# Kernel optimization log

Hardware: AMD Instinct MI355X
Metric: run time of the kernel (lower is better)

The kernel has to match this reference:

```python
import jax, jax.numpy as jnp
import numpy as np

N_NODES = 50000
N_EDGES = 800000
IN_F, HID, EMB = 10, 256, 128
BN_EPS = 1e-5


def _glorot(key, shape):
    fan_in, fan_out = shape[0], shape[1]
    lim = (6.0 / (fan_in + fan_out)) ** 0.5
    return jax.random.uniform(key, shape, jnp.float32, -lim, lim)


def setup_inputs() -> dict:
    key = jax.random.key(0)
    ks = jax.random.split(key, 16)
    inp = {
        "x": jax.random.normal(ks[0], (N_NODES, IN_F), jnp.float32),
        "edge_index": jax.random.randint(ks[1], (2, N_EDGES), 0, N_NODES, jnp.int64),
        # input_proj: Linear(10,256) + BN
        "w_in": _glorot(ks[2], (IN_F, HID)),
        "b_in": jnp.zeros((HID,), jnp.float32),
        "g_in": jnp.ones((HID,), jnp.float32),
        "be_in": jnp.zeros((HID,), jnp.float32),
        # SAGEConv 1 (256->256): lin_l (neighbor aggr, with bias), lin_r (root, no bias)
        "wl1": _glorot(ks[3], (HID, HID)), "bl1": jnp.zeros((HID,), jnp.float32), "wr1": _glorot(ks[4], (HID, HID)),
        "g1": jnp.ones((HID,), jnp.float32), "be1": jnp.zeros((HID,), jnp.float32),
        # SAGEConv 2 (256->256)
        "wl2": _glorot(ks[5], (HID, HID)), "bl2": jnp.zeros((HID,), jnp.float32), "wr2": _glorot(ks[6], (HID, HID)),
        "g2": jnp.ones((HID,), jnp.float32), "be2": jnp.zeros((HID,), jnp.float32),
        # SAGEConv 3 (256->128)
        "wl3": _glorot(ks[7], (HID, EMB)), "bl3": jnp.zeros((EMB,), jnp.float32), "wr3": _glorot(ks[8], (HID, EMB)),
    }
    return inp


def _bn(h, g, b):
    # BatchNorm1d in training-mode math (batch statistics, biased variance)
    mu = jnp.mean(h, axis=0)
    var = jnp.var(h, axis=0)
    return (h - mu) * jax.lax.rsqrt(var + BN_EPS) * g + b


def _sage(h, src, dst, wl, bl, wr):
    # mean aggregation of neighbor messages: gather h[src], scatter-mean into dst
    msg = h[src]                                             # [E, d]
    s = jax.ops.segment_sum(msg, dst, num_segments=N_NODES)  # [N, d]
    cnt = jax.ops.segment_sum(jnp.ones((msg.shape[0],), h.dtype), dst, num_segments=N_NODES)
    agg = s / jnp.maximum(cnt, 1.0)[:, None]                 # isolated nodes -> 0
    return agg @ wl + bl + h @ wr


def reference(x, edge_index, w_in, b_in, g_in, be_in,
              wl1, bl1, wr1, g1, be1,
              wl2, bl2, wr2, g2, be2,
              wl3, bl3, wr3):
    src, dst = edge_index[0], edge_index[1]
    # input_proj: Linear + BN + ReLU (dropout disabled for determinism)
    h = jax.nn.relu(_bn(x @ w_in + b_in, g_in, be_in))
    h = jax.nn.relu(_bn(_sage(h, src, dst, wl1, bl1, wr1), g1, be1))
    h = jax.nn.relu(_bn(_sage(h, src, dst, wl2, bl2, wr2), g2, be2))
    h = _sage(h, src, dst, wl3, bl3, wr3)
    return h
```

## Files before the change

### kernel.cpp

```cpp
#include <hip/hip_runtime.h>

#define N_NODES 50000
#define N_EDGES 800000
#define IN_F 10
#define HID 256
#define EMB 128
#define BN_EPS 1e-5f
#define N_SCAN_BLKS ((N_NODES + 255) / 256)
#define CNT_BLKS (N_EDGES / 256)
#define WCONV_ELEMS (4 * HID * HID + 2 * EMB * HID)
#define WCONV_BLKS (WCONV_ELEMS / 256)
#define SSTRIDE 512
#define NSHARD 8
#define NPART 8
#define PART_SZ (N_NODES / NPART)
#define SCAT_BLKS 2048

typedef __attribute__((ext_vector_type(8))) short short8;
typedef __attribute__((ext_vector_type(4))) float floatx4;
typedef __attribute__((ext_vector_type(2))) float floatx2;

__device__ __forceinline__ unsigned short f2bf(float f) {
    unsigned u = __float_as_uint(f);
    unsigned r = (u + 0x7fffu + ((u >> 16) & 1u)) >> 16;
    return (unsigned short)r;
}
__device__ __forceinline__ float bf_lo(unsigned int u) { return __uint_as_float(u << 16); }
__device__ __forceinline__ float bf_hi(unsigned int u) { return __uint_as_float(u & 0xffff0000u); }
__device__ __forceinline__ float bf2f(unsigned short s) { return __uint_as_float(((unsigned)s) << 16); }

__device__ __forceinline__ void gload_lds16(const unsigned short* g, unsigned short* l) {
    __builtin_amdgcn_global_load_lds(
        (const __attribute__((address_space(1))) unsigned int*)(uintptr_t)(const void*)g,
        (__attribute__((address_space(3))) unsigned int*)(unsigned int)(uintptr_t)(void*)l,
        16, 0, 0);
}

__global__ void k_count_wconv(const int* __restrict__ e_dst, int* __restrict__ cnt,
                              const float* __restrict__ wl1, const float* __restrict__ wr1,
                              const float* __restrict__ wl2, const float* __restrict__ wr2,
                              const float* __restrict__ wl3, const float* __restrict__ wr3,
                              unsigned short* __restrict__ wl1t, unsigned short* __restrict__ wr1t,
                              unsigned short* __restrict__ wl2t, unsigned short* __restrict__ wr2t,
                              unsigned short* __restrict__ wl3t, unsigned short* __restrict__ wr3t) {
    int b = blockIdx.x;
    int t = threadIdx.x;
    if (b < CNT_BLKS) {
        atomicAdd(&cnt[e_dst[b * 256 + t]], 1);
        return;
    }
    int idx = (b - CNT_BLKS) * 256 + t;
    const int S = HID * HID;
    if (idx < 4 * S) {
        int sel = idx >> 16;
        int o = idx & (S - 1);
        const float* w = sel == 0 ? wl1 : sel == 1 ? wr1 : sel == 2 ? wl2 : wr2;
        unsigned short* wt = sel == 0 ? wl1t : sel == 1 ? wr1t : sel == 2 ? wl2t : wr2t;
        int n = o >> 8, k = o & 255;
        wt[o] = f2bf(w[k * HID + n]);
    } else {
        int r = idx - 4 * S;
        int sel = r >> 15;
        int o = r & 32767;
        const float* w = sel ? wr3 : wl3;
        unsigned short* wt = sel ? wr3t : wl3t;
        int n = o >> 8, k = o & 255;
        wt[o] = f2bf(w[k * EMB + n]);
    }
}

__global__ void k_reduce_cnt(const int* __restrict__ cnt, int* __restrict__ part) {
    __shared__ int sdata[256];
    int i = blockIdx.x * 256 + threadIdx.x;
    sdata[threadIdx.x] = (i < N_NODES) ? cnt[i] : 0;
    __syncthreads();
    for (int off = 128; off > 0; off >>= 1) {
        if (threadIdx.x < off) sdata[threadIdx.x] += sdata[threadIdx.x + off];
        __syncthreads();
    }
    if (threadIdx.x == 0) part[blockIdx.x] = sdata[0];
}

__global__ void k_scan_part(const int* __restrict__ part, int* __restrict__ partoff,
                            int* __restrict__ row_off_last) {
    __shared__ int buf[256];
    int tid = threadIdx.x;
    int v = (tid < N_SCAN_BLKS) ? part[tid] : 0;
    buf[tid] = v;
    __syncthreads();
    for (int off = 1; off < 256; off <<= 1) {
        int t = (tid >= off) ? buf[tid - off] : 0;
        __syncthreads();
        buf[tid] += t;
        __syncthreads();
    }
    if (tid < N_SCAN_BLKS) partoff[tid] = buf[tid] - v;
    if (tid == 255) *row_off_last = buf[255];
}

__global__ void k_scan_final(const int* __restrict__ cnt, const int* __restrict__ partoff,
                             int* __restrict__ row_off, int* __restrict__ fill_pos) {
    __shared__ int buf[256];
    int tid = threadIdx.x;
    int i = blockIdx.x * 256 + tid;
    int v = (i < N_NODES) ? cnt[i] : 0;
    buf[tid] = v;
    __syncthreads();
    for (int off = 1; off < 256; off <<= 1) {
        int t = (tid >= off) ? buf[tid - off] : 0;
        __syncthreads();
        buf[tid] += t;
        __syncthreads();
    }
    if (i < N_NODES) {
        int excl = partoff[blockIdx.x] + buf[tid] - v;
        row_off[i] = excl;
        fill_pos[i] = excl;
    }
}

__global__ void k_scatter_part(const int* __restrict__ src, const int* __restrict__ dst,
                               int* __restrict__ fill_pos, int* __restrict__ sorted_src) {
    int part = blockIdx.x & 7;
    int lo = part * PART_SZ, hi = lo + PART_SZ;
    int idx = (blockIdx.x >> 3) * 256 + threadIdx.x;
    for (int e = idx; e < N_EDGES; e += (SCAT_BLKS / 8) * 256) {
        int d = dst[e];
        if (d >= lo && d < hi) {
            int p = atomicAdd(&fill_pos[d], 1);
            sorted_src[p] = src[e];
        }
    }
}

#define IP_BLOCKS 1024
__global__ __launch_bounds__(256) void k_input_proj(
        const float* __restrict__ x, const float* __restrict__ w,
        const float* __restrict__ bias, unsigned short* __restrict__ h,
        float* __restrict__ stats) {
    __shared__ float sbuf[2048];
    __shared__ float qbuf[2048];
    int t = threadIdx.x;
    int jg = t & 31;
    int ns = t >> 5;
    int j0 = jg * 8;

    float wreg[IN_F][8];
#pragma unroll
    for (int k = 0; k < IN_F; k++)
#pragma unroll
        for (int c = 0; c < 8; c++) wreg[k][c] = w[k * HID + j0 + c];
    float bj[8];
#pragma unroll
    for (int c = 0; c < 8; c++) bj[c] = bias[j0 + c];

    float s[8] = {}, q[8] = {};
    const int stride = IP_BLOCKS * 8;
    for (int base = blockIdx.x * 8 + ns; base < N_NODES; base += stride) {
        float xr[IN_F];
#pragma unroll
        for (int k = 0; k < IN_F; k++) xr[k] = x[base * IN_F + k];
        float acc[8];
#pragma unroll
        for (int c = 0; c < 8; c++) {
            float a = bj[c];
#pragma unroll
            for (int k = 0; k < IN_F; k++) a += xr[k] * wreg[k][c];
            acc[c] = a;
            s[c] += a;
            q[c] += a * a;
        }
        uint4 o;
        o.x = (unsigned)f2bf(acc[0]) | ((unsigned)f2bf(acc[1]) << 16);
        o.y = (unsigned)f2bf(acc[2]) | ((unsigned)f2bf(acc[3]) << 16);
        o.z = (unsigned)f2bf(acc[4]) | ((unsigned)f2bf(acc[5]) << 16);
        o.w = (unsigned)f2bf(acc[6]) | ((unsigned)f2bf(acc[7]) << 16);
        ((uint4*)h)[(size_t)base * 32 + jg] = o;
    }

#pragma unroll
    for (int c = 0; c < 8; c++) {
        sbuf[ns * 256 + j0 + c] = s[c];
        qbuf[ns * 256 + j0 + c] = q[c];
    }
    __syncthreads();
    float ss = 0.f, qq = 0.f;
#pragma unroll
    for (int n2 = 0; n2 < 8; n2++) {
        ss += sbuf[n2 * 256 + t];
        qq += qbuf[n2 * 256 + t];
    }
    atomicAdd(&stats[t], ss);
    atomicAdd(&stats[256 + t], qq);
}

__global__ void k_bn_apply_relu(unsigned short* __restrict__ h, const float* __restrict__ stats,
                                const float* __restrict__ g, const float* __restrict__ b,
                                unsigned char* __restrict__ h8) {
    int idx = blockIdx.x * 256 + threadIdx.x;
    if (idx >= N_NODES * 32) return;
    int q = idx & 31;
    int j0 = q * 8;
    const float invn = 1.0f / (float)N_NODES;
    float sc[8], sh[8];
#pragma unroll
    for (int k = 0; k < 8; k++) {
        float ssum = 0.f, qsum = 0.f;
#pragma unroll
        for (int s = 0; s < NSHARD; s++) {
            ssum += stats[s * SSTRIDE + j0 + k];
            qsum += stats[s * SSTRIDE + 256 + j0 + k];
        }
        float mu = ssum * invn;
        float var = qsum * invn - mu * mu;
        float scale = g[j0 + k] * rsqrtf(var + BN_EPS);
        sc[k] = scale;
        sh[k] = b[j0 + k] - mu * scale;
    }
    uint4 v = ((uint4*)h)[idx];
    float f0 = fmaxf(bf_lo(v.x) * sc[0] + sh[0], 0.f);
    float f1 = fmaxf(bf_hi(v.x) * sc[1] + sh[1], 0.f);
    float f2 = fmaxf(bf_lo(v.y) * sc[2] + sh[2], 0.f);
    float f3 = fmaxf(bf_hi(v.y) * sc[3] + sh[3], 0.f);
    float f4 = fmaxf(bf_lo(v.z) * sc[4] + sh[4], 0.f);
    float f5 = fmaxf(bf_hi(v.z) * sc[5] + sh[5], 0.f);
    float f6 = fmaxf(bf_lo(v.w) * sc[6] + sh[6], 0.f);
    float f7 = fmaxf(bf_hi(v.w) * sc[7] + sh[7], 0.f);
    uint4 o;
    o.x = (unsigned)f2bf(f0) | ((unsigned)f2bf(f1) << 16);
    o.y = (unsigned)f2bf(f2) | ((unsigned)f2bf(f3) << 16);
    o.z = (unsigned)f2bf(f4) | ((unsigned)f2bf(f5) << 16);
    o.w = (unsigned)f2bf(f6) | ((unsigned)f2bf(f7) << 16);
    ((uint4*)h)[idx] = o;
    if (h8) {
        unsigned pa = __builtin_amdgcn_cvt_pk_fp8_f32(f0, f1, 0u, false);
        pa = __builtin_amdgcn_cvt_pk_fp8_f32(f2, f3, pa, true);
        unsigned pb = __builtin_amdgcn_cvt_pk_fp8_f32(f4, f5, 0u, false);
        pb = __builtin_amdgcn_cvt_pk_fp8_f32(f6, f7, pb, true);
        uint2 o8; o8.x = pa; o8.y = pb;
        ((uint2*)h8)[idx] = o8;
    }
}

__global__ void k_aggregate_fp8(const unsigned char* __restrict__ h8,
                                const int* __restrict__ row_off, const int* __restrict__ cnt,
                                const int* __restrict__ sorted_src,
                                unsigned short* __restrict__ agg) {
    int node = (blockIdx.x * blockDim.x + threadIdx.x) >> 4;
    int lane = threadIdx.x & 15;
    if (node >= N_NODES) return;
    int beg = row_off[node];
    int d = cnt[node];
    int end = beg + d;
    const uint4* h4 = (const uint4*)h8;
    float a[16] = {};
    for (int e = beg; e < end; e++) {
        int s = sorted_src[e];
        uint4 v = h4[(size_t)s * 16 + lane];
        floatx2 p;
        p = __builtin_amdgcn_cvt_pk_f32_fp8(v.x, false); a[0] += p.x;  a[1] += p.y;
        p = __builtin_amdgcn_cvt_pk_f32_fp8(v.x, true);  a[2] += p.x;  a[3] += p.y;
        p = __builtin_amdgcn_cvt_pk_f32_fp8(v.y, false); a[4] += p.x;  a[5] += p.y;
        p = __builtin_amdgcn_cvt_pk_f32_fp8(v.y, true);  a[6] += p.x;  a[7] += p.y;
        p = __builtin_amdgcn_cvt_pk_f32_fp8(v.z, false); a[8] += p.x;  a[9] += p.y;
        p = __builtin_amdgcn_cvt_pk_f32_fp8(v.z, true);  a[10] += p.x; a[11] += p.y;
        p = __builtin_amdgcn_cvt_pk_f32_fp8(v.w, false); a[12] += p.x; a[13] += p.y;
        p = __builtin_amdgcn_cvt_pk_f32_fp8(v.w, true);  a[14] += p.x; a[15] += p.y;
    }
    float inv = 1.0f / (float)(d > 1 ? d : 1);
    uint4 o0, o1;
    o0.x = (unsigned)f2bf(a[0] * inv)  | ((unsigned)f2bf(a[1] * inv) << 16);
    o0.y = (unsigned)f2bf(a[2] * inv)  | ((unsigned)f2bf(a[3] * inv) << 16);
    o0.z = (unsigned)f2bf(a[4] * inv)  | ((unsigned)f2bf(a[5] * inv) << 16);
    o0.w = (unsigned)f2bf(a[6] * inv)  | ((unsigned)f2bf(a[7] * inv) << 16);
    o1.x = (unsigned)f2bf(a[8] * inv)  | ((unsigned)f2bf(a[9] * inv) << 16);
    o1.y = (unsigned)f2bf(a[10] * inv) | ((unsigned)f2bf(a[11] * inv) << 16);
    o1.z = (unsigned)f2bf(a[12] * inv) | ((unsigned)f2bf(a[13] * inv) << 16);
    o1.w = (unsigned)f2bf(a[14] * inv) | ((unsigned)f2bf(a[15] * inv) << 16);
    ((uint4*)agg)[(size_t)node * 32 + lane * 2] = o0;
    ((uint4*)agg)[(size_t)node * 32 + lane * 2 + 1] = o1;
}

__global__ void k_aggregate_add(const unsigned short* __restrict__ G, const int* __restrict__ row_off,
                                const int* __restrict__ cnt, const int* __restrict__ sorted_src,
                                float* __restrict__ out) {
    int node = (blockIdx.x * blockDim.x + threadIdx.x) >> 4;
    int lane = threadIdx.x & 15;
    if (node >= N_NODES) return;
    int beg = row_off[node];
    int d = cnt[node];
    int end = beg + d;
    const uint4* h4 = (const uint4*)G;
    float a0 = 0.f, a1 = 0.f, a2 = 0.f, a3 = 0.f, a4 = 0.f, a5 = 0.f, a6 = 0.f, a7 = 0.f;
    for (int e = beg; e < end; e++) {
        int s = sorted_src[e];
        uint4 v = h4[(size_t)s * 16 + lane];
        a0 += bf_lo(v.x); a1 += bf_hi(v.x);
        a2 += bf_lo(v.y); a3 += bf_hi(v.y);
        a4 += bf_lo(v.z); a5 += bf_hi(v.z);
        a6 += bf_lo(v.w); a7 += bf_hi(v.w);
    }
    float inv = 1.0f / (float)(d > 1 ? d : 1);
    float4* ob = (float4*)(out + (size_t)node * EMB + lane * 8);
    float4 p0 = ob[0], p1 = ob[1];
    p0.x += a0 * inv; p0.y += a1 * inv; p0.z += a2 * inv; p0.w += a3 * inv;
    p1.x += a4 * inv; p1.y += a5 * inv; p1.z += a6 * inv; p1.w += a7 * inv;
    ob[0] = p0; ob[1] = p1;
}

#define BK 64

#define GEMM_BLKS 784

template <int NCOL, bool STATS>
__global__ __launch_bounds__(512, 4) void k_gemm_mfma(
        const unsigned short* __restrict__ A1, const unsigned short* __restrict__ B1t,
        const unsigned short* __restrict__ A2, const unsigned short* __restrict__ B2t,
        const float* __restrict__ bias, float* __restrict__ stats,
        unsigned short* __restrict__ Cout) {
    int b = blockIdx.x;
    int xcd = b & 7;
    int q = b >> 3;
    int cx = q & 1;
    int pr = (q >> 1) * 8 + xcd;
    int r0 = pr * 128;
    if (r0 >= N_NODES) return;
    int c0 = cx * 128;

    __shared__ __attribute__((aligned(16))) unsigned short As[2][128 * 64];
    __shared__ __attribute__((aligned(16))) unsigned short Bs[2][128 * 64];

    int t = threadIdx.x;
    int wave = t >> 6, lane = t & 63;
    int wm = wave >> 2, wn = wave & 3;
    int quad = lane >> 4, l15 = lane & 15;

    floatx4 acc[4][2];
#pragma unroll
    for (int i = 0; i < 4; i++)
#pragma unroll
        for (int j = 0; j < 2; j++) acc[i][j] = (floatx4){0.f, 0.f, 0.f, 0.f};

    auto stage = [&](int buf, const unsigned short* __restrict__ A,
                     const unsigned short* __restrict__ B, int k0) {
#pragma unroll
        for (int it = 0; it < 2; it++) {
            int p = it * 512 + t;
            int row = p >> 3, ps = p & 7;
            int ls = ps ^ (row & 7);
            int rr = r0 + row;
            if (rr >= N_NODES) rr = N_NODES - 1;
            gload_lds16(&A[(size_t)rr * HID + k0 + ls * 8], &As[buf][p * 8]);
        }
#pragma unroll
        for (int it = 0; it < 2; it++) {
            int p = it * 512 + t;
            int row = p >> 3, ps = p & 7;
            int ls = ps ^ (row & 7);
            gload_lds16(&B[(size_t)(c0 + row) * HID + k0 + ls * 8], &Bs[buf][p * 8]);
        }
    };

    stage(0, A1, B1t, 0);

    int cur = 0;
#pragma unroll
    for (int ph = 0; ph < 8; ph++) {
        if (ph < 7) {
            int np = ph + 1;
            stage(cur ^ 1, (np >= 4) ? A2 : A1, (np >= 4) ? B2t : B1t, (np & 3) * BK);
            asm volatile("s_waitcnt vmcnt(4)\n\ts_barrier" ::: "memory");
        } else {
            asm volatile("s_waitcnt vmcnt(0)\n\ts_barrier" ::: "memory");
        }
#pragma unroll
        for (int kc = 0; kc < 2; kc++) {
            short8 a[4], bfr[2];
            int ls = kc * 4 + quad;
#pragma unroll
            for (int i = 0; i < 4; i++) {
                int arow = wm * 64 + i * 16 + l15;
                int ps = ls ^ (arow & 7);
                a[i] = *(const short8*)&As[cur][arow * 64 + ps * 8];
            }
#pragma unroll
            for (int j = 0; j < 2; j++) {
                int brow = wn * 32 + j * 16 + l15;
                int ps = ls ^ (brow & 7);
                bfr[j] = *(const short8*)&Bs[cur][brow * 64 + ps * 8];
            }
            __builtin_amdgcn_s_setprio(1);
#pragma unroll
            for (int i = 0; i < 4; i++)
#pragma unroll
                for (int j = 0; j < 2; j++)
                    acc[i][j] = __builtin_amdgcn_mfma_f32_16x16x32_bf16(a[i], bfr[j], acc[i][j], 0, 0, 0);
            __builtin_amdgcn_s_setprio(0);
        }
        asm volatile("s_barrier" ::: "memory");
        cur ^= 1;
    }

    float bv[2];
#pragma unroll
    for (int j = 0; j < 2; j++) bv[j] = bias[c0 + wn * 32 + j * 16 + l15];

    float s_part[2] = {0.f, 0.f};
    float q_part[2] = {0.f, 0.f};

#pragma unroll
    for (int i = 0; i < 4; i++) {
#pragma unroll
        for (int r = 0; r < 4; r++) {
            int m = r0 + wm * 64 + i * 16 + quad * 4 + r;
            if (m >= N_NODES) continue;
#pragma unroll
            for (int j = 0; j < 2; j++) {
                int n = c0 + wn * 32 + j * 16 + l15;
                float v = acc[i][j][r] + bv[j];
                if (STATS) { s_part[j] += v; q_part[j] += v * v; }
                Cout[(size_t)m * NCOL + n] = f2bf(v);
            }
        }
    }

    if (STATS) {
        float* sred = (float*)As;
        __syncthreads();
        if (t < 256) sred[t] = 0.f;
        __syncthreads();
#pragma unroll
        for (int j = 0; j < 2; j++) {
            int cl = wn * 32 + j * 16 + l15;
            atomicAdd(&sred[cl], s_part[j]);
            atomicAdd(&sred[128 + cl], q_part[j]);
        }
        __syncthreads();
        if (t < 128) {
            int base = (pr & (NSHARD - 1)) * SSTRIDE;
            atomicAdd(&stats[base + c0 + t], sred[t]);
            atomicAdd(&stats[base + 256 + c0 + t], sred[128 + t]);
        }
    }
}

#define L3_BLKS 784

__global__ __launch_bounds__(512, 4) void k_gemm_l3_dual(
        const unsigned short* __restrict__ A, const unsigned short* __restrict__ Bt,
        const float* __restrict__ stats,
        const float* __restrict__ g, const float* __restrict__ be,
        const float* __restrict__ bl3, unsigned short* __restrict__ G,
        float* __restrict__ P) {
    int b = blockIdx.x;
    int xcd = b & 7;
    int q = b >> 3;
    int cx = q & 1;
    int pr = (q >> 1) * 8 + xcd;
    int r0 = pr * 128;
    if (r0 >= N_NODES) return;
    int c0 = cx * 128;

    __shared__ __attribute__((aligned(16))) unsigned short As[128 * 64];
    __shared__ __attribute__((aligned(16))) unsigned short Bs[2][128 * 64];
    __shared__ float scs[256], shs[256];

    int t = threadIdx.x;
    if (t < 256) {
        const float invn = 1.0f / (float)N_NODES;
        float ssum = 0.f, qsum = 0.f;
#pragma unroll
        for (int s = 0; s < NSHARD; s++) {
            ssum += stats[s * SSTRIDE + t];
            qsum += stats[s * SSTRIDE + 256 + t];
        }
        float mu = ssum * invn;
        float var = qsum * invn - mu * mu;
        float sc = g[t] * rsqrtf(var + BN_EPS);
        scs[t] = sc;
        shs[t] = be[t] - mu * sc;
    }
    __syncthreads();

    int wave = t >> 6, lane = t & 63;
    int wm = wave >> 2, wn = wave & 3;
    int quad = lane >> 4, l15 = lane & 15;

    floatx4 acc[4][2];
#pragma unroll
    for (int i = 0; i < 4; i++)
#pragma unroll
        for (int j = 0; j < 2; j++) acc[i][j] = (floatx4){0.f, 0.f, 0.f, 0.f};

    int p0_ = t, p1_ = 512 + t;
    int row0 = p0_ >> 3, ps0 = p0_ & 7, ls0 = ps0 ^ (row0 & 7);
    int row1 = p1_ >> 3, ps1 = p1_ & 7, ls1 = ps1 ^ (row1 & 7);
    int ar0 = r0 + row0; if (ar0 >= N_NODES) ar0 = N_NODES - 1;
    int ar1 = r0 + row1; if (ar1 >= N_NODES) ar1 = N_NODES - 1;

    auto stageB = [&](int buf, int k0) {
        gload_lds16(&Bt[(size_t)(c0 + row0) * HID + k0 + ls0 * 8], &Bs[buf][p0_ * 8]);
        gload_lds16(&Bt[(size_t)(c0 + row1) * HID + k0 + ls1 * 8], &Bs[buf][p1_ * 8]);
    };
    auto issueA = [&](int k0, uint4& v0, uint4& v1) {
        v0 = *(const uint4*)&A[(size_t)ar0 * HID + k0 + ls0 * 8];
        v1 = *(const uint4*)&A[(size_t)ar1 * HID + k0 + ls1 * 8];
    };
    auto xform = [&](uint4 vv, int cb) -> uint4 {
        float4 s0 = *(float4*)&scs[cb], s1 = *(float4*)&scs[cb + 4];
        float4 h0 = *(float4*)&shs[cb], h1 = *(float4*)&shs[cb + 4];
        float f0 = fmaxf(bf_lo(vv.x) * s0.x + h0.x, 0.f);
        float f1 = fmaxf(bf_hi(vv.x) * s0.y + h0.y, 0.f);
        float f2 = fmaxf(bf_lo(vv.y) * s0.z + h0.z, 0.f);
        float f3 = fmaxf(bf_hi(vv.y) * s0.w + h0.w, 0.f);
        float f4 = fmaxf(bf_lo(vv.z) * s1.x + h1.x, 0.f);
        float f5 = fmaxf(bf_hi(vv.z) * s1.y + h1.y, 0.f);
        float f6 = fmaxf(bf_lo(vv.w) * s1.z + h1.z, 0.f);
        float f7 = fmaxf(bf_hi(vv.w) * s1.w + h1.w, 0.f);
        uint4 ov;
        ov.x = (unsigned)f2bf(f0) | ((unsigned)f2bf(f1) << 16);
        ov.y = (unsigned)f2bf(f2) | ((unsigned)f2bf(f3) << 16);
        ov.z = (unsigned)f2bf(f4) | ((unsigned)f2bf(f5) << 16);
        ov.w = (unsigned)f2bf(f6) | ((unsigned)f2bf(f7) << 16);
        return ov;
    };

    uint4 va0, va1, vb0, vb1;
    stageB(0, 0);
    issueA(0, va0, va1);

    int cur = 0;
#pragma unroll
    for (int ph = 0; ph < 4; ph++) {
        if (ph < 3) {
            stageB(cur ^ 1, (ph + 1) * BK);
            asm volatile("s_waitcnt vmcnt(2)" ::: "memory");
        } else {
            asm volatile("s_waitcnt vmcnt(0)" ::: "memory");
        }
        *(uint4*)&As[p0_ * 8] = xform(va0, ph * BK + ls0 * 8);
        *(uint4*)&As[p1_ * 8] = xform(va1, ph * BK + ls1 * 8);
        asm volatile("s_waitcnt lgkmcnt(0)\n\ts_barrier" ::: "memory");
        if (ph < 3) issueA((ph + 1) * BK, vb0, vb1);
#pragma unroll
        for (int kc = 0; kc < 2; kc++) {
            short8 a[4], bfr[2];
            int ls = kc * 4 + quad;
#pragma unroll
            for (int i = 0; i < 4; i++) {
                int arow = wm * 64 + i * 16 + l15;
                int ps = ls ^ (arow & 7);
                a[i] = *(const short8*)&As[arow * 64 + ps * 8];
            }
#pragma unroll
            for (int j = 0; j < 2; j++) {
                int brow = wn * 32 + j * 16 + l15;
                int ps = ls ^ (brow & 7);
                bfr[j] = *(const short8*)&Bs[cur][brow * 64 + ps * 8];
            }
            __builtin_amdgcn_s_setprio(1);
#pragma unroll
            for (int i = 0; i < 4; i++)
#pragma unroll
                for (int j = 0; j < 2; j++)
                    acc[i][j] = __builtin_amdgcn_mfma_f32_16x16x32_bf16(a[i], bfr[j], acc[i][j], 0, 0, 0);
            __builtin_amdgcn_s_setprio(0);
        }
        asm volatile("s_barrier" ::: "memory");
        cur ^= 1;
        va0 = vb0; va1 = vb1;
    }

    float bv[2];
#pragma unroll
    for (int j = 0; j < 2; j++) bv[j] = bl3[wn * 32 + j * 16 + l15];

#pragma unroll
    for (int i = 0; i < 4; i++) {
#pragma unroll
        for (int r = 0; r < 4; r++) {
            int m = r0 + wm * 64 + i * 16 + quad * 4 + r;
            if (m >= N_NODES) continue;
#pragma unroll
            for (int j = 0; j < 2; j++) {
                int n = wn * 32 + j * 16 + l15;
                if (cx == 0) G[(size_t)m * EMB + n] = f2bf(acc[i][j][r]);
                else         P[(size_t)m * EMB + n] = acc[i][j][r] + bv[j];
            }
        }
    }
}

extern "C" void kernel_launch(void* const* d_in, const int* in_sizes, int n_in,
                              void* d_out, int out_size, void* d_ws, size_t ws_size,
                              hipStream_t stream) {
    const float* x    = (const float*)d_in[0];
    const int*   ei   = (const int*)d_in[1];
    const float* w_in = (const float*)d_in[2];
    const float* b_in = (const float*)d_in[3];
    const float* g_in = (const float*)d_in[4];
    const float* be_in= (const float*)d_in[5];
    const float* wl1  = (const float*)d_in[6];
    const float* bl1  = (const float*)d_in[7];
    const float* wr1  = (const float*)d_in[8];
    const float* g1   = (const float*)d_in[9];
    const float* be1  = (const float*)d_in[10];
    const float* wl2  = (const float*)d_in[11];
    const float* bl2  = (const float*)d_in[12];
    const float* wr2  = (const float*)d_in[13];
    const float* g2   = (const float*)d_in[14];
    const float* be2  = (const float*)d_in[15];
    const float* wl3  = (const float*)d_in[16];
    const float* bl3  = (const float*)d_in[17];
    const float* wr3  = (const float*)d_in[18];
    float* out = (float*)d_out;

    char* p = (char*)d_ws;
    auto alloc = [&](size_t bytes) -> void* {
        void* r = (void*)p;
        p += (bytes + 255) & ~(size_t)255;
        return r;
    };
    int*   cnt    = (int*)alloc((size_t)N_NODES * 4);
    float* stats0 = (float*)alloc((size_t)NSHARD * SSTRIDE * 4);
    float* stats1 = (float*)alloc((size_t)NSHARD * SSTRIDE * 4);
    float* stats2 = (float*)alloc((size_t)NSHARD * SSTRIDE * 4);
    size_t zlen = (size_t)((char*)stats2 + NSHARD * SSTRIDE * 4 - (char*)cnt);

    unsigned short* bufA = (unsigned short*)alloc((size_t)N_NODES * HID * 2);
    unsigned short* bufB = (unsigned short*)alloc((size_t)N_NODES * HID * 2);
    unsigned short* bufC = (unsigned short*)alloc((size_t)N_NODES * HID * 2);
    unsigned char*  h8   = (unsigned char*)alloc((size_t)N_NODES * HID);
    unsigned short* wl1t = (unsigned short*)alloc((size_t)HID * HID * 2);
    unsigned short* wr1t = (unsigned short*)alloc((size_t)HID * HID * 2);
    unsigned short* wl2t = (unsigned short*)alloc((size_t)HID * HID * 2);
    unsigned short* wr2t = (unsigned short*)alloc((size_t)HID * HID * 2);
    unsigned short* wl3t = (unsigned short*)alloc((size_t)EMB * HID * 2);
    unsigned short* wr3t = (unsigned short*)alloc((size_t)EMB * HID * 2);
    int*   row_off    = (int*)alloc((size_t)(N_NODES + 1) * 4);
    int*   fill_pos   = (int*)alloc((size_t)N_NODES * 4);
    int*   sorted_src = (int*)alloc((size_t)N_EDGES * 4);
    int*   part       = (int*)alloc((size_t)256 * 4);
    int*   partoff    = (int*)alloc((size_t)256 * 4);
    (void)wr3t;

    const int* e_src = ei;
    const int* e_dst = ei + N_EDGES;

    hipMemsetAsync(cnt, 0, zlen, stream);
    k_count_wconv<<<CNT_BLKS + WCONV_BLKS, 256, 0, stream>>>(
        e_dst, cnt, wl1, wr1, wl2, wr2, wl3, wr3, wl1t, wr1t, wl2t, wr2t, wl3t, wr3t);
    k_reduce_cnt<<<N_SCAN_BLKS, 256, 0, stream>>>(cnt, part);
    k_scan_part<<<1, 256, 0, stream>>>(part, partoff, &row_off[N_NODES]);
    k_scan_final<<<N_SCAN_BLKS, 256, 0, stream>>>(cnt, partoff, row_off, fill_pos);
    k_scatter_part<<<SCAT_BLKS, 256, 0, stream>>>(e_src, e_dst, fill_pos, sorted_src);

    k_input_proj<<<IP_BLOCKS, 256, 0, stream>>>(x, w_in, b_in, bufA, stats0);
    k_bn_apply_relu<<<(N_NODES * 32 + 255) / 256, 256, 0, stream>>>(bufA, stats0, g_in, be_in, h8);

    int aggF8_blocks = (N_NODES * 16 + 255) / 256;

    k_aggregate_fp8<<<aggF8_blocks, 256, 0, stream>>>(h8, row_off, cnt, sorted_src, bufC);
    k_gemm_mfma<HID, true><<<GEMM_BLKS, 512, 0, stream>>>(bufC, wl1t, bufA, wr1t, bl1, stats1, bufB);
    k_bn_apply_relu<<<(N_NODES * 32 + 255) / 256, 256, 0, stream>>>(bufB, stats1, g1, be1, h8);

    k_aggregate_fp8<<<aggF8_blocks, 256, 0, stream>>>(h8, row_off, cnt, sorted_src, bufC);
    k_gemm_mfma<HID, true><<<GEMM_BLKS, 512, 0, stream>>>(bufC, wl2t, bufB, wr2t, bl2, stats2, bufA);

    k_gemm_l3_dual<<<L3_BLKS, 512, 0, stream>>>(
        bufA, wl3t, stats2, g2, be2, bl3, bufB, out);
    k_aggregate_add<<<(N_NODES * 16 + 255) / 256, 256, 0, stream>>>(bufB, row_off, cnt, sorted_src, out);
}
```

Baseline: 486.1 us.

## Split aggregation edges across four lane groups and fuse input projection into count kernel

The aggregation kernels now assign a full 64-lane wavefront per node, with four 16-lane groups each handling every fourth edge, and combine the partial sums with cross-lane shuffles. This raises memory-level parallelism for the gathers over an average degree of 16 and spreads work more evenly across nodes with different degrees. Separately, the input projection is folded into the edge-count and weight-conversion launch as extra blocks, removing one kernel launch and letting that work overlap with the counting. The cost is four times as many threads per node, some of them idle for low-degree nodes, plus the shuffle reduction.

```diff
diff --git a/kernel.cpp b/kernel.cpp
--- a/kernel.cpp
+++ b/kernel.cpp
@@ -10,6 +10,7 @@
 #define CNT_BLKS (N_EDGES / 256)
 #define WCONV_ELEMS (4 * HID * HID + 2 * EMB * HID)
 #define WCONV_BLKS (WCONV_ELEMS / 256)
+#define IP_BLOCKS 1024
 #define SSTRIDE 512
 #define NSHARD 8
 #define NPART 8
@@ -36,37 +37,98 @@
         16, 0, 0);
 }
 
-__global__ void k_count_wconv(const int* __restrict__ e_dst, int* __restrict__ cnt,
-                              const float* __restrict__ wl1, const float* __restrict__ wr1,
-                              const float* __restrict__ wl2, const float* __restrict__ wr2,
-                              const float* __restrict__ wl3, const float* __restrict__ wr3,
-                              unsigned short* __restrict__ wl1t, unsigned short* __restrict__ wr1t,
-                              unsigned short* __restrict__ wl2t, unsigned short* __restrict__ wr2t,
-                              unsigned short* __restrict__ wl3t, unsigned short* __restrict__ wr3t) {
+__global__ __launch_bounds__(256) void k_count_wconv_ip(
+        const int* __restrict__ e_dst, int* __restrict__ cnt,
+        const float* __restrict__ wl1, const float* __restrict__ wr1,
+        const float* __restrict__ wl2, const float* __restrict__ wr2,
+        const float* __restrict__ wl3, const float* __restrict__ wr3,
+        unsigned short* __restrict__ wl1t, unsigned short* __restrict__ wr1t,
+        unsigned short* __restrict__ wl2t, unsigned short* __restrict__ wr2t,
+        unsigned short* __restrict__ wl3t, unsigned short* __restrict__ wr3t,
+        const float* __restrict__ x, const float* __restrict__ w,
+        const float* __restrict__ bias, unsigned short* __restrict__ h,
+        float* __restrict__ stats) {
+    __shared__ float sbuf[2048];
+    __shared__ float qbuf[2048];
     int b = blockIdx.x;
     int t = threadIdx.x;
     if (b < CNT_BLKS) {
         atomicAdd(&cnt[e_dst[b * 256 + t]], 1);
         return;
     }
-    int idx = (b - CNT_BLKS) * 256 + t;
-    const int S = HID * HID;
-    if (idx < 4 * S) {
-        int sel = idx >> 16;
-        int o = idx & (S - 1);
-        const float* w = sel == 0 ? wl1 : sel == 1 ? wr1 : sel == 2 ? wl2 : wr2;
-        unsigned short* wt = sel == 0 ? wl1t : sel == 1 ? wr1t : sel == 2 ? wl2t : wr2t;
-        int n = o >> 8, k = o & 255;
-        wt[o] = f2bf(w[k * HID + n]);
-    } else {
-        int r = idx - 4 * S;
-        int sel = r >> 15;
-        int o = r & 32767;
-        const float* w = sel ? wr3 : wl3;
-        unsigned short* wt = sel ? wr3t : wl3t;
-        int n = o >> 8, k = o & 255;
-        wt[o] = f2bf(w[k * EMB + n]);
-    }
+    if (b < CNT_BLKS + WCONV_BLKS) {
+        int idx = (b - CNT_BLKS) * 256 + t;
+        const int S = HID * HID;
+        if (idx < 4 * S) {
+            int sel = idx >> 16;
+            int o = idx & (S - 1);
+            const float* wp = sel == 0 ? wl1 : sel == 1 ? wr1 : sel == 2 ? wl2 : wr2;
+            unsigned short* wt = sel == 0 ? wl1t : sel == 1 ? wr1t : sel == 2 ? wl2t : wr2t;
+            int n = o >> 8, k = o & 255;
+            wt[o] = f2bf(wp[k * HID + n]);
+        } else {
+            int r = idx - 4 * S;
+            int sel = r >> 15;
+            int o = r & 32767;
+            const float* wp = sel ? wr3 : wl3;
+            unsigned short* wt = sel ? wr3t : wl3t;
+            int n = o >> 8, k = o & 255;
+            wt[o] = f2bf(wp[k * EMB + n]);
+        }
+        return;
+    }
+    int bb = b - CNT_BLKS - WCONV_BLKS;
+    int jg = t & 31;
+    int ns = t >> 5;
+    int j0 = jg * 8;
+
+    float wreg[IN_F][8];
+#pragma unroll
+    for (int k = 0; k < IN_F; k++)
+#pragma unroll
+        for (int c = 0; c < 8; c++) wreg[k][c] = w[k * HID + j0 + c];
+    float bj[8];
+#pragma unroll
+    for (int c = 0; c < 8; c++) bj[c] = bias[j0 + c];
+
+    float s[8] = {}, q[8] = {};
+    const int stride = IP_BLOCKS * 8;
+    for (int base = bb * 8 + ns; base < N_NODES; base += stride) {
+        float xr[IN_F];
+#pragma unroll
+        for (int k = 0; k < IN_F; k++) xr[k] = x[base * IN_F + k];
+        float acc[8];
+#pragma unroll
+        for (int c = 0; c < 8; c++) {
+            float a = bj[c];
+#pragma unroll
+            for (int k = 0; k < IN_F; k++) a += xr[k] * wreg[k][c];
+            acc[c] = a;
+            s[c] += a;
+            q[c] += a * a;
+        }
+        uint4 o;
+        o.x = (unsigned)f2bf(acc[0]) | ((unsigned)f2bf(acc[1]) << 16);
+        o.y = (unsigned)f2bf(acc[2]) | ((unsigned)f2bf(acc[3]) << 16);
+        o.z = (unsigned)f2bf(acc[4]) | ((unsigned)f2bf(acc[5]) << 16);
+        o.w = (unsigned)f2bf(acc[6]) | ((unsigned)f2bf(acc[7]) << 16);
+        ((uint4*)h)[(size_t)base * 32 + jg] = o;
+    }
+
+#pragma unroll
+    for (int c = 0; c < 8; c++) {
+        sbuf[ns * 256 + j0 + c] = s[c];
+        qbuf[ns * 256 + j0 + c] = q[c];
+    }
+    __syncthreads();
+    float ss = 0.f, qq = 0.f;
+#pragma unroll
+    for (int n2 = 0; n2 < 8; n2++) {
+        ss += sbuf[n2 * 256 + t];
+        qq += qbuf[n2 * 256 + t];
+    }
+    atomicAdd(&stats[t], ss);
+    atomicAdd(&stats[256 + t], qq);
 }
 
 __global__ void k_reduce_cnt(const int* __restrict__ cnt, int* __restrict__ part) {
@@ -131,67 +193,6 @@
             sorted_src[p] = src[e];
         }
     }
-}
-
-#define IP_BLOCKS 1024
-__global__ __launch_bounds__(256) void k_input_proj(
-        const float* __restrict__ x, const float* __restrict__ w,
-        const float* __restrict__ bias, unsigned short* __restrict__ h,
-        float* __restrict__ stats) {
-    __shared__ float sbuf[2048];
-    __shared__ float qbuf[2048];
-    int t = threadIdx.x;
-    int jg = t & 31;
-    int ns = t >> 5;
-    int j0 = jg * 8;
-
-    float wreg[IN_F][8];
-#pragma unroll
-    for (int k = 0; k < IN_F; k++)
-#pragma unroll
-        for (int c = 0; c < 8; c++) wreg[k][c] = w[k * HID + j0 + c];
-    float bj[8];
-#pragma unroll
-    for (int c = 0; c < 8; c++) bj[c] = bias[j0 + c];
-
-    float s[8] = {}, q[8] = {};
-    const int stride = IP_BLOCKS * 8;
-    for (int base = blockIdx.x * 8 + ns; base < N_NODES; base += stride) {
-        float xr[IN_F];
-#pragma unroll
-        for (int k = 0; k < IN_F; k++) xr[k] = x[base * IN_F + k];
-        float acc[8];
-#pragma unroll
-        for (int c = 0; c < 8; c++) {
-            float a = bj[c];
-#pragma unroll
-            for (int k = 0; k < IN_F; k++) a += xr[k] * wreg[k][c];
-            acc[c] = a;
-            s[c] += a;
-            q[c] += a * a;
-        }
-        uint4 o;
-        o.x = (unsigned)f2bf(acc[0]) | ((unsigned)f2bf(acc[1]) << 16);
-        o.y = (unsigned)f2bf(acc[2]) | ((unsigned)f2bf(acc[3]) << 16);
-        o.z = (unsigned)f2bf(acc[4]) | ((unsigned)f2bf(acc[5]) << 16);
-        o.w = (unsigned)f2bf(acc[6]) | ((unsigned)f2bf(acc[7]) << 16);
-        ((uint4*)h)[(size_t)base * 32 + jg] = o;
-    }
-
-#pragma unroll
-    for (int c = 0; c < 8; c++) {
-        sbuf[ns * 256 + j0 + c] = s[c];
-        qbuf[ns * 256 + j0 + c] = q[c];
-    }
-    __syncthreads();
-    float ss = 0.f, qq = 0.f;
-#pragma unroll
-    for (int n2 = 0; n2 < 8; n2++) {
-        ss += sbuf[n2 * 256 + t];
-        qq += qbuf[n2 * 256 + t];
-    }
-    atomicAdd(&stats[t], ss);
-    atomicAdd(&stats[256 + t], qq);
 }
 
 __global__ void k_bn_apply_relu(unsigned short* __restrict__ h, const float* __restrict__ stats,
@@ -246,15 +247,16 @@
                                 const int* __restrict__ row_off, const int* __restrict__ cnt,
                                 const int* __restrict__ sorted_src,
                                 unsigned short* __restrict__ agg) {
-    int node = (blockIdx.x * blockDim.x + threadIdx.x) >> 4;
-    int lane = threadIdx.x & 15;
+    int node = (blockIdx.x * blockDim.x + threadIdx.x) >> 6;
+    int l = threadIdx.x & 63;
+    int ec = l >> 4;
+    int lane = l & 15;
     if (node >= N_NODES) return;
     int beg = row_off[node];
     int d = cnt[node];
-    int end = beg + d;
     const uint4* h4 = (const uint4*)h8;
     float a[16] = {};
-    for (int e = beg; e < end; e++) {
+    for (int e = beg + ec; e < beg + d; e += 4) {
         int s = sorted_src[e];
         uint4 v = h4[(size_t)s * 16 + lane];
         floatx2 p;
@@ -267,6 +269,12 @@
         p = __builtin_amdgcn_cvt_pk_f32_fp8(v.w, false); a[12] += p.x; a[13] += p.y;
         p = __builtin_amdgcn_cvt_pk_f32_fp8(v.w, true);  a[14] += p.x; a[15] += p.y;
     }
+#pragma unroll
+    for (int i = 0; i < 16; i++) {
+        a[i] += __shfl_xor(a[i], 32, 64);
+        a[i] += __shfl_xor(a[i], 16, 64);
+    }
+    if (ec) return;
     float inv = 1.0f / (float)(d > 1 ? d : 1);
     uint4 o0, o1;
     o0.x = (unsigned)f2bf(a[0] * inv)  | ((unsigned)f2bf(a[1] * inv) << 16);
@@ -284,15 +292,16 @@
 __global__ void k_aggregate_add(const unsigned short* __restrict__ G, const int* __restrict__ row_off,
                                 const int* __restrict__ cnt, const int* __restrict__ sorted_src,
                                 float* __restrict__ out) {
-    int node = (blockIdx.x * blockDim.x + threadIdx.x) >> 4;
-    int lane = threadIdx.x & 15;
+    int node = (blockIdx.x * blockDim.x + threadIdx.x) >> 6;
+    int l = threadIdx.x & 63;
+    int ec = l >> 4;
+    int lane = l & 15;
     if (node >= N_NODES) return;
     int beg = row_off[node];
     int d = cnt[node];
-    int end = beg + d;
     const uint4* h4 = (const uint4*)G;
     float a0 = 0.f, a1 = 0.f, a2 = 0.f, a3 = 0.f, a4 = 0.f, a5 = 0.f, a6 = 0.f, a7 = 0.f;
-    for (int e = beg; e < end; e++) {
+    for (int e = beg + ec; e < beg + d; e += 4) {
         int s = sorted_src[e];
         uint4 v = h4[(size_t)s * 16 + lane];
         a0 += bf_lo(v.x); a1 += bf_hi(v.x);
@@ -300,11 +309,18 @@
         a4 += bf_lo(v.z); a5 += bf_hi(v.z);
         a6 += bf_lo(v.w); a7 += bf_hi(v.w);
     }
+    float r[8] = {a0, a1, a2, a3, a4, a5, a6, a7};
+#pragma unroll
+    for (int i = 0; i < 8; i++) {
+        r[i] += __shfl_xor(r[i], 32, 64);
+        r[i] += __shfl_xor(r[i], 16, 64);
+    }
+    if (ec) return;
     float inv = 1.0f / (float)(d > 1 ? d : 1);
     float4* ob = (float4*)(out + (size_t)node * EMB + lane * 8);
     float4 p0 = ob[0], p1 = ob[1];
-    p0.x += a0 * inv; p0.y += a1 * inv; p0.z += a2 * inv; p0.w += a3 * inv;
-    p1.x += a4 * inv; p1.y += a5 * inv; p1.z += a6 * inv; p1.w += a7 * inv;
+    p0.x += r[0] * inv; p0.y += r[1] * inv; p0.z += r[2] * inv; p0.w += r[3] * inv;
+    p1.x += r[4] * inv; p1.y += r[5] * inv; p1.z += r[6] * inv; p1.w += r[7] * inv;
     ob[0] = p0; ob[1] = p1;
 }
 
@@ -648,26 +664,26 @@
     const int* e_dst = ei + N_EDGES;
 
     hipMemsetAsync(cnt, 0, zlen, stream);
-    k_count_wconv<<<CNT_BLKS + WCONV_BLKS, 256, 0, stream>>>(
-        e_dst, cnt, wl1, wr1, wl2, wr2, wl3, wr3, wl1t, wr1t, wl2t, wr2t, wl3t, wr3t);
+    k_count_wconv_ip<<<CNT_BLKS + WCONV_BLKS + IP_BLOCKS, 256, 0, stream>>>(
+        e_dst, cnt, wl1, wr1, wl2, wr2, wl3, wr3, wl1t, wr1t, wl2t, wr2t, wl3t, wr3t,
+        x, w_in, b_in, bufA, stats0);
     k_reduce_cnt<<<N_SCAN_BLKS, 256, 0, stream>>>(cnt, part);
     k_scan_part<<<1, 256, 0, stream>>>(part, partoff, &row_off[N_NODES]);
     k_scan_final<<<N_SCAN_BLKS, 256, 0, stream>>>(cnt, partoff, row_off, fill_pos);
     k_scatter_part<<<SCAT_BLKS, 256, 0, stream>>>(e_src, e_dst, fill_pos, sorted_src);
 
-    k_input_proj<<<IP_BLOCKS, 256, 0, stream>>>(x, w_in, b_in, bufA, stats0);
     k_bn_apply_relu<<<(N_NODES * 32 + 255) / 256, 256, 0, stream>>>(bufA, stats0, g_in, be_in, h8);
 
-    int aggF8_blocks = (N_NODES * 16 + 255) / 256;
-
-    k_aggregate_fp8<<<aggF8_blocks, 256, 0, stream>>>(h8, row_off, cnt, sorted_src, bufC);
+    int agg_blocks = ((size_t)N_NODES * 64 + 255) / 256;
+
+    k_aggregate_fp8<<<agg_blocks, 256, 0, stream>>>(h8, row_off, cnt, sorted_src, bufC);
     k_gemm_mfma<HID, true><<<GEMM_BLKS, 512, 0, stream>>>(bufC, wl1t, bufA, wr1t, bl1, stats1, bufB);
     k_bn_apply_relu<<<(N_NODES * 32 + 255) / 256, 256, 0, stream>>>(bufB, stats1, g1, be1, h8);
 
-    k_aggregate_fp8<<<aggF8_blocks, 256, 0, stream>>>(h8, row_off, cnt, sorted_src, bufC);
+    k_aggregate_fp8<<<agg_blocks, 256, 0, stream>>>(h8, row_off, cnt, sorted_src, bufC);
     k_gemm_mfma<HID, true><<<GEMM_BLKS, 512, 0, stream>>>(bufC, wl2t, bufB, wr2t, bl2, stats2, bufA);
 
     k_gemm_l3_dual<<<L3_BLKS, 512, 0, stream>>>(
         bufA, wl3t, stats2, g2, be2, bl3, bufB, out);
-    k_aggregate_add<<<(N_NODES * 16 + 255) / 256, 256, 0, stream>>>(bufB, row_off, cnt, sorted_src, out);
-}
+    k_aggregate_add<<<agg_blocks, 256, 0, stream>>>(bufB, row_off, cnt, sorted_src, out);
+}
```

Result: no change. 488.5 us (+0.5%).
